# Kernel tuning notes

Measured on AMD Instinct MI355X. Metric: run time of the kernel, lower is better.

The kernel has to match this reference:

```python
import jax, jax.numpy as jnp
import numpy as np
import math

NH = 16
SIGMA = 1.5
KS = 7


def _gaussian_blur_16x16(x):
    # x: (N, 16, 16); torchvision GaussianBlur(7, 1.5) with reflect padding
    hx = jnp.arange(KS, dtype=x.dtype) - (KS - 1) / 2.0
    k1 = jnp.exp(-0.5 * (hx / SIGMA) ** 2)
    k1 = k1 / k1.sum()
    k2 = jnp.outer(k1, k1)[None, None]  # (1,1,7,7)
    pad = KS // 2
    xp = jnp.pad(x, ((0, 0), (pad, pad), (pad, pad)), mode='reflect')[:, None]
    y = jax.lax.conv_general_dilated(xp, k2, (1, 1), 'VALID')
    return y[:, 0]


def _normalize(w):
    mn, mx = w.min(), w.max()
    return (w - mn) / (mx - mn)


def _blurred_map(f, b_perm):
    # f, b_perm: (B, 256, 256)
    B = f.shape[0]
    bi = f * b_perm
    bi = bi.reshape(B * 256, 16, 16)
    bl = _gaussian_blur_16x16(bi)
    bl = jnp.clip(_normalize(bl), 0.0, 1.0)
    bl = bl.reshape(B, 256, 256)
    return bl * f * b_perm


def setup_inputs() -> dict:
    key = jax.random.key(0)
    ks = jax.random.split(key, 16)
    B, T, C = 4, 827, 1024
    inp = {
        'x': jax.random.normal(ks[0], (B, T, C), jnp.float32),
        'h': jax.random.normal(ks[1], (B, NH, 827, 827), jnp.float32) * 0.1,
        'f01': jax.random.uniform(ks[2], (B, 256, 256), jnp.float32),
        'f02': jax.random.uniform(ks[3], (B, 256, 256), jnp.float32),
        'f12': jax.random.uniform(ks[4], (B, 256, 256), jnp.float32),
        'b01': jax.random.uniform(ks[5], (B, 256, 256), jnp.float32),
        'b02': jax.random.uniform(ks[6], (B, 256, 256), jnp.float32),
        'b12': jax.random.uniform(ks[7], (B, 256, 256), jnp.float32),
        'Wq': jax.random.normal(ks[8], (C, C), jnp.float32) * 0.02,
        'bq': jnp.zeros((C,), jnp.float32),
        'Wk': jax.random.normal(ks[9], (C, C), jnp.float32) * 0.02,
        'bk': jnp.zeros((C,), jnp.float32),
        'Wv': jax.random.normal(ks[10], (C, C), jnp.float32) * 0.02,
        'bv': jnp.zeros((C,), jnp.float32),
        'Wp': jax.random.normal(ks[11], (C, C), jnp.float32) * 0.02,
        'bp': jnp.zeros((C,), jnp.float32),
    }
    return inp


def reference(x, h, f01, f02, f12, b01, b02, b12,
              Wq, bq, Wk, bk, Wv, bv, Wp, bp):
    B, T, C = x.shape
    hd = C // NH
    # QKV projections -> (B, NH, T, hd)
    def proj(W, b):
        return (x @ W + b).reshape(B, T, NH, hd).transpose(0, 2, 1, 3)
    q, k, v = proj(Wq, bq), proj(Wk, bk), proj(Wv, bv)

    att = jnp.einsum('bhtd,bhsd->bhts', q, k) * (1.0 / math.sqrt(hd))
    att = h[:, :, :T, :T] + att  # adaptive additive bias

    # bidirectional epipolar multiplicative masks with blur
    b01p = jnp.transpose(b01, (0, 2, 1))
    b02p = jnp.transpose(b02, (0, 2, 1))
    b12p = jnp.transpose(b12, (0, 2, 1))
    blur01 = _blurred_map(f01, b01p)[:, None]  # (B,1,256,256), broadcast over heads
    blur02 = _blurred_map(f02, b02p)[:, None]
    blur12 = _blurred_map(f12, b12p)[:, None]

    n1 = min(T - 285, 256)
    att = att.at[:, :, 285:285 + n1, 0:256].multiply(blur01[:, :, :n1])
    if T > 571:
        n2 = T - 571
        att = att.at[:, :, 571:T, 0:256].multiply(blur02[:, :, :n2])
        att = att.at[:, :, 571:T, 286:542].multiply(blur12[:, :, :n2])

    mask = jnp.tril(jnp.ones((T, T), dtype=bool))
    att = jnp.where(mask, att, -jnp.inf)
    att = jax.nn.softmax(att, axis=-1)

    y = jnp.einsum('bhts,bhsd->bhtd', att, v)
    y = y.transpose(0, 2, 1, 3).reshape(B, T, C)
    return y @ Wp + bp
```

## Files before the change

### kernel.cpp

```cpp
#include <hip/hip_runtime.h>
#include <math.h>

using bfrag8 = __attribute__((ext_vector_type(8))) short;
using facc4  = __attribute__((ext_vector_type(4))) float;

#define MFMA16(a,b,c) __builtin_amdgcn_mfma_f32_16x16x32_bf16((a),(b),(c),0,0,0)

#define T_SEQ 827
#define T_PAD 832
#define NHEAD 16
#define NEG_INF (-__builtin_inff())
#define CM_TOT 1179392

static __device__ __forceinline__ unsigned short f2bf(float f) {
    unsigned int x = __float_as_uint(f);
    unsigned int r = x + 0x7FFFu + ((x >> 16) & 1u);
    return (unsigned short)(r >> 16);
}

static __device__ __forceinline__ void gl16(const unsigned short* g, unsigned short* l) {
    __builtin_amdgcn_global_load_lds(
        (const __attribute__((address_space(1))) unsigned int*)g,
        (__attribute__((address_space(3))) unsigned int*)l,
        16, 0, 0);
}

__global__ __launch_bounds__(256) void k_front(const float* __restrict__ x,
                                               unsigned short* __restrict__ x_bf,
                                               float* __restrict__ cm,
                                               unsigned short* q, unsigned short* k,
                                               unsigned short* vT,
                                               const float* __restrict__ Wq,
                                               const float* __restrict__ Wk,
                                               const float* __restrict__ Wv,
                                               const float* __restrict__ Wp,
                                               unsigned short* __restrict__ Wt_out,
                                               const float* f01, const float* f02, const float* f12,
                                               const float* b01, const float* b02, const float* b12,
                                               float* __restrict__ bl,
                                               float* __restrict__ pmm) {
    __shared__ float tile[32][33];
    __shared__ float img[16][17], tmp[16][17];
    __shared__ float smn[4], smx[4];
    int bid = blockIdx.x, tid = threadIdx.x;

    if (bid < 3308) {
        int i = (bid * 256 + tid) * 4;
        float4 v = *reinterpret_cast<const float4*>(x + i);
        ushort4 o;
        o.x = f2bf(v.x); o.y = f2bf(v.y); o.z = f2bf(v.z); o.w = f2bf(v.w);
        *reinterpret_cast<ushort4*>(x_bf + i) = o;
    } else if (bid < 4460) {
        int base = (bid - 3308) * 1024 + tid * 4;
        if (base + 4 <= CM_TOT) {
            float4 one = {1.f, 1.f, 1.f, 1.f};
            *reinterpret_cast<float4*>(cm + base) = one;
        } else {
#pragma unroll
            for (int j = 0; j < 4; ++j)
                if (base + j < CM_TOT) cm[base + j] = 1.f;
        }
    } else if (bid < 4524) {
        int bh = bid - 4460;
        for (int i = tid; i < 320; i += 256) {
            int t = 827 + i / 64, d = i % 64;
            q[((size_t)bh * T_PAD + t) * 64 + d] = 0;
            k[((size_t)bh * T_PAD + t) * 64 + d] = 0;
        }
        for (int i = tid; i < 4096; i += 256) {
            int d = i >> 6, s = 768 + (i & 63);
            vT[((size_t)bh * 64 + d) * T_PAD + s] = 0;
        }
    } else if (bid < 8620) {
        int i = bid - 4524;
        int z = i >> 10, rem = i & 1023;
        int bx = rem & 31, by = rem >> 5;
        const float* W = (z == 0) ? Wq : (z == 1) ? Wk : (z == 2) ? Wv : Wp;
        unsigned short* Wt = Wt_out + (size_t)z * 1048576;
        int tx = tid & 31, ty0 = tid >> 5;
#pragma unroll
        for (int j = 0; j < 4; ++j) {
            int ty = ty0 + j * 8;
            tile[ty][tx] = W[(size_t)(by * 32 + ty) * 1024 + bx * 32 + tx];
        }
        __syncthreads();
#pragma unroll
        for (int j = 0; j < 4; ++j) {
            int ty = ty0 + j * 8;
            Wt[(size_t)(bx * 32 + ty) * 1024 + by * 32 + tx] = f2bf(tile[tx][ty]);
        }
    } else {
        int i = bid - 8620;
        int m = i >> 10, rem = i & 1023, b = rem >> 8, r = rem & 255;
        const float* f  = (m == 0) ? f01 : (m == 1) ? f02 : f12;
        const float* bm = (m == 0) ? b01 : (m == 1) ? b02 : b12;
        int ii = tid >> 4, j = tid & 15;

        float k1[7]; float ks = 0.f;
#pragma unroll
        for (int d = 0; d < 7; ++d) { float hx = (float)d - 3.f; k1[d] = expf(-0.5f * hx * hx / 2.25f); ks += k1[d]; }
#pragma unroll
        for (int d = 0; d < 7; ++d) k1[d] /= ks;

        size_t idx = (size_t)b * 65536 + (size_t)r * 256 + tid;
        float bi = f[idx] * bm[(size_t)b * 65536 + (size_t)tid * 256 + r];
        img[ii][j] = bi;
        __syncthreads();
        float ha = 0.f;
#pragma unroll
        for (int d = 0; d < 7; ++d) { int p = j - 3 + d; p = p < 0 ? -p : (p > 15 ? 30 - p : p); ha += k1[d] * img[ii][p]; }
        tmp[ii][j] = ha;
        __syncthreads();
        float v = 0.f;
#pragma unroll
        for (int d = 0; d < 7; ++d) { int p = ii - 3 + d; p = p < 0 ? -p : (p > 15 ? 30 - p : p); v += k1[d] * tmp[p][j]; }
        bl[(size_t)m * 262144 + idx] = v;

        float mn = v, mx = v;
#pragma unroll
        for (int off = 32; off; off >>= 1) { mn = fminf(mn, __shfl_xor(mn, off)); mx = fmaxf(mx, __shfl_xor(mx, off)); }
        int wid = tid >> 6, lane = tid & 63;
        if (lane == 0) { smn[wid] = mn; smx[wid] = mx; }
        __syncthreads();
        if (tid == 0) {
            mn = fminf(fminf(smn[0], smn[1]), fminf(smn[2], smn[3]));
            mx = fmaxf(fmaxf(smx[0], smx[1]), fmaxf(smx[2], smx[3]));
            pmm[2 * i]     = mn;
            pmm[2 * i + 1] = mx;
        }
    }
}

__global__ __launch_bounds__(256) void k_gemm_qkv(const unsigned short* __restrict__ A,
                                              const unsigned short* __restrict__ Bt,
                                              const float* __restrict__ b0, const float* __restrict__ b1,
                                              const float* __restrict__ b2,
                                              unsigned short* __restrict__ qo, unsigned short* __restrict__ ko,
                                              unsigned short* __restrict__ vo, int M,
                                              const float* f01, const float* f02, const float* f12,
                                              const float* b01, const float* b02, const float* b12,
                                              const float* __restrict__ bl,
                                              const float* __restrict__ pmm,
                                              float* __restrict__ cm) {
    __shared__ unsigned short As[2][4096];
    __shared__ unsigned short Bs[2][4096];
    int bid = blockIdx.x, tid = threadIdx.x;

    if (bid >= 624) {
        int i = bid - 624;
        int m = i >> 10, rem = i & 1023, b = rem >> 8, r = rem & 255;
        float mn = __builtin_inff(), mx = 0.f;
        for (int kk = tid; kk < 1024; kk += 256) {
            int e = m * 1024 + kk;
            mn = fminf(mn, pmm[2 * e]);
            mx = fmaxf(mx, pmm[2 * e + 1]);
        }
#pragma unroll
        for (int off = 32; off; off >>= 1) { mn = fminf(mn, __shfl_xor(mn, off)); mx = fmaxf(mx, __shfl_xor(mx, off)); }
        float* fs = reinterpret_cast<float*>(&As[0][0]);
        int wid = tid >> 6, lane = tid & 63;
        if (lane == 0) { fs[wid] = mn; fs[4 + wid] = mx; }
        __syncthreads();
        mn = fminf(fminf(fs[0], fs[1]), fminf(fs[2], fs[3]));
        mx = fmaxf(fmaxf(fs[4], fs[5]), fmaxf(fs[6], fs[7]));

        const float* f  = (m == 0) ? f01 : (m == 1) ? f02 : f12;
        const float* bm = (m == 0) ? b01 : (m == 1) ? b02 : b12;
        size_t idx = (size_t)b * 65536 + (size_t)r * 256 + tid;
        float w = (bl[(size_t)m * 262144 + idx] - mn) / (mx - mn);
        w = fminf(fmaxf(w, 0.f), 1.f);
        float val = w * f[idx] * bm[(size_t)b * 65536 + (size_t)tid * 256 + r];
        int row = (m == 0) ? r : r + 286;
        int col = (m == 2) ? tid + 286 : tid;
        cm[((size_t)b * 542 + row) * 544 + col] = val;
        return;
    }

    int swz = (bid & 7) * 78 + (bid >> 3);
    int m0 = (swz % 26) * 128, n0 = (swz / 26) * 128;
    int wid = tid >> 6, lane = tid & 63;
    int g = lane >> 4, l15 = lane & 15;
    int wm = wid >> 1, wn = wid & 1;
    facc4 acc[4][4] = {};

    int ar0 = m0 + (tid >> 2); if (ar0 > M - 1) ar0 = M - 1;
    int ar1 = m0 + 64 + (tid >> 2); if (ar1 > M - 1) ar1 = M - 1;
    const unsigned short* Ap0 = A + (size_t)ar0 * 1024 + (tid & 3) * 8;
    const unsigned short* Ap1 = A + (size_t)ar1 * 1024 + (tid & 3) * 8;
    const unsigned short* Bp0 = Bt + (size_t)(n0 + (tid >> 2)) * 1024 + (tid & 3) * 8;
    const unsigned short* Bp1 = Bp0 + (size_t)64 * 1024;

    auto stage = [&](int koff, int buf) {
        gl16(Ap0 + koff, &As[buf][0] + (wid << 9));
        gl16(Ap1 + koff, &As[buf][0] + (wid << 9) + 2048);
        gl16(Bp0 + koff, &Bs[buf][0] + (wid << 9));
        gl16(Bp1 + koff, &Bs[buf][0] + (wid << 9) + 2048);
    };

    stage(0, 0);
    for (int k0 = 0; k0 < 32; ++k0) {
        int cur = k0 & 1;
        bool morek = (k0 + 1 < 32);
        if (morek) {
            stage((k0 + 1) * 32, cur ^ 1);
            asm volatile("s_waitcnt vmcnt(4)" ::: "memory");
        } else {
            asm volatile("s_waitcnt vmcnt(0)" ::: "memory");
        }
        __builtin_amdgcn_s_barrier();
        __builtin_amdgcn_sched_barrier(0);

        bfrag8 af[4], bf[4];
#pragma unroll
        for (int mi = 0; mi < 4; ++mi)
            af[mi] = *reinterpret_cast<const bfrag8*>(&As[cur][(wm * 64 + mi * 16 + l15) * 32 + g * 8]);
#pragma unroll
        for (int ni = 0; ni < 4; ++ni)
            bf[ni] = *reinterpret_cast<const bfrag8*>(&Bs[cur][(wn * 64 + ni * 16 + l15) * 32 + g * 8]);
        __builtin_amdgcn_s_setprio(1);
#pragma unroll
        for (int mi = 0; mi < 4; ++mi)
#pragma unroll
            for (int ni = 0; ni < 4; ++ni)
                acc[mi][ni] = MFMA16(af[mi], bf[ni], acc[mi][ni]);
        __builtin_amdgcn_s_setprio(0);

        __builtin_amdgcn_sched_barrier(0);
        if (morek) __builtin_amdgcn_s_barrier();
    }

    int which = n0 >> 10;
    const float* bb = (which == 0 ? b0 : (which == 1 ? b1 : b2));
#pragma unroll
    for (int mi = 0; mi < 4; ++mi)
#pragma unroll
        for (int ni = 0; ni < 4; ++ni)
#pragma unroll
            for (int r = 0; r < 4; ++r) {
                int row = m0 + wm * 64 + mi * 16 + g * 4 + r;
                if (row >= M) continue;
                int col = n0 + wn * 64 + ni * 16 + l15;
                float v = acc[mi][ni][r] + bb[col & 1023];
                int b = row / T_SEQ, t = row - b * T_SEQ;
                int cc = col & 1023;
                int hh = cc >> 6, d = cc & 63;
                size_t bh = (size_t)(b * NHEAD + hh);
                if (which == 0) {
                    qo[(bh * T_PAD + t) * 64 + d] = f2bf(v);
                } else if (which == 1) {
                    int du = (((d >> 3) ^ (t & 7)) << 3) | (d & 7);
                    ko[(bh * T_PAD + t) * 64 + du] = f2bf(v);
                } else {
                    int sl = t & 63;
                    int su = (((sl >> 3) ^ (d & 7)) << 3) | (t & 7);
                    vo[(bh * 64 + d) * T_PAD + (t - sl) + su] = f2bf(v);
                }
            }
}

__global__ __launch_bounds__(256) void k_proj64(const unsigned short* __restrict__ A,
                                                const unsigned short* __restrict__ Bt,
                                                const float* __restrict__ bias,
                                                float* __restrict__ out, int M) {
    __shared__ unsigned short As[2048];
    __shared__ unsigned short Bs[2048];
    int bid = blockIdx.x, tid = threadIdx.x;
    int swz = (bid & 7) * 104 + (bid >> 3);
    int m0 = (swz % 52) * 64, n0 = (swz / 52) * 64;
    int wid = tid >> 6, lane = tid & 63;
    int g = lane >> 4, l15 = lane & 15;
    int wm = wid >> 1, wn = wid & 1;
    facc4 acc[2][2] = {};

    int ar = m0 + (tid >> 2); if (ar > M - 1) ar = M - 1;
    const unsigned short* Ap = A + (size_t)ar * 1024 + (tid & 3) * 8;
    const unsigned short* Bp = Bt + (size_t)(n0 + (tid >> 2)) * 1024 + (tid & 3) * 8;
    unsigned short* asw = As + (wid << 9);
    unsigned short* bsw = Bs + (wid << 9);

    for (int k0 = 0; k0 < 1024; k0 += 32) {
        if (k0) __syncthreads();
        gl16(Ap + k0, asw);
        gl16(Bp + k0, bsw);
        __syncthreads();
        bfrag8 af[2], bf[2];
#pragma unroll
        for (int mi = 0; mi < 2; ++mi)
            af[mi] = *reinterpret_cast<const bfrag8*>(&As[(wm * 32 + mi * 16 + l15) * 32 + g * 8]);
#pragma unroll
        for (int ni = 0; ni < 2; ++ni)
            bf[ni] = *reinterpret_cast<const bfrag8*>(&Bs[(wn * 32 + ni * 16 + l15) * 32 + g * 8]);
#pragma unroll
        for (int mi = 0; mi < 2; ++mi)
#pragma unroll
            for (int ni = 0; ni < 2; ++ni)
                acc[mi][ni] = MFMA16(af[mi], bf[ni], acc[mi][ni]);
    }

#pragma unroll
    for (int mi = 0; mi < 2; ++mi)
#pragma unroll
        for (int ni = 0; ni < 2; ++ni)
#pragma unroll
            for (int r = 0; r < 4; ++r) {
                int row = m0 + wm * 32 + mi * 16 + g * 4 + r;
                if (row >= M) continue;
                int col = n0 + wn * 32 + ni * 16 + l15;
                out[(size_t)row * 1024 + col] = acc[mi][ni][r] + bias[col];
            }
}

__global__ __launch_bounds__(256, 3) void k_attn(const unsigned short* __restrict__ qb,
                                              const unsigned short* __restrict__ kb,
                                              const unsigned short* __restrict__ vT,
                                              const float* __restrict__ h,
                                              const float* __restrict__ cm,
                                              unsigned short* __restrict__ y) {
    int blk0 = blockIdx.x;
    int blk = (blk0 & 7) * 104 + (blk0 >> 3);
    int bh = blk / 13;
    int qt = 12 - (blk % 13);
    int b = bh >> 4, hh = bh & 15;
    int tid = threadIdx.x, wid = tid >> 6, lane = tid & 63;
    int g = lane >> 4, l15 = lane & 15;
    int t0 = qt * 64 + wid * 16;
    int t = t0 + l15;
    int tcl = t > 826 ? 826 : t;
    int ntiles = qt + 1;

    __shared__ unsigned short Ks[2][4096];
    __shared__ unsigned short Vs[2][4096];
    __shared__ unsigned short Ps[4][1024];
    unsigned short* pw = &Ps[wid][0];

    const unsigned short* Kbase = kb + (size_t)bh * T_PAD * 64;
    const unsigned short* Vbase = vT + (size_t)bh * 64 * T_PAD;
    const float* hrow = h + (size_t)bh * T_SEQ * T_SEQ + (size_t)tcl * T_SEQ;
    int rt = t - 285; rt = rt < 0 ? 0 : (rt > 541 ? 541 : rt);
    const float* cmrow = cm + ((size_t)b * 542 + rt) * 544;
    bool tm = (t >= 285);

    size_t qrow = ((size_t)bh * T_PAD + t) * 64 + g * 8;
    bfrag8 aq0 = *reinterpret_cast<const bfrag8*>(qb + qrow);
    bfrag8 aq1 = *reinterpret_cast<const bfrag8*>(qb + qrow + 32);

    auto stage = [&](int s0, int buf) {
        const unsigned short* kt = Kbase + (size_t)s0 * 64;
        unsigned short* kd = &Ks[buf][0] + (wid << 9);
        gl16(kt + tid * 8, kd);
        gl16(kt + 2048 + tid * 8, kd + 2048);
        const unsigned short* vt = Vbase + s0;
        unsigned short* vd = &Vs[buf][0] + (wid << 9);
        gl16(vt + (size_t)(tid >> 3) * T_PAD + (tid & 7) * 8, vd);
        gl16(vt + (size_t)((tid >> 3) + 32) * T_PAD + (tid & 7) * 8, vd + 2048);
    };

    auto loadh_h = [&](int s0t, float* hd) {
#pragma unroll
        for (int nt = 0; nt < 4; ++nt) {
            int sb = s0t + nt * 16 + 4 * g;
#pragma unroll
            for (int j = 0; j < 4; ++j) {
                int a = sb + j;
                int ac = a > 826 ? 826 : a;
                float hx = hrow[ac];
                hd[nt * 4 + j] = (a <= tcl) ? hx : 0.f;
            }
        }
    };

    auto loadm = [&](int s0t, float* mvd) {
#pragma unroll
        for (int nt = 0; nt < 4; ++nt) {
            int sb = s0t + nt * 16 + 4 * g;
            float m4[4];
            if (tm && sb <= 540) {
                __builtin_memcpy(m4, cmrow + sb, 16);
            } else {
#pragma unroll
                for (int j = 0; j < 4; ++j) m4[j] = 1.f;
            }
#pragma unroll
            for (int j = 0; j < 4; ++j) mvd[nt * 4 + j] = m4[j];
        }
    };

    float m_r = NEG_INF, l_r = 0.f;
    facc4 acc[4] = {};
    float hv[16], mv[16], hn[16];
    stage(0, 0);
    loadh_h(0, hv);
    loadm(0, mv);

    for (int it = 0; it < ntiles; ++it) {
        int cur = it & 1, s0 = it * 64;
        bool more = (it + 1 < ntiles);
        bool diag = !more;

        if (more) {
            stage(s0 + 64, cur ^ 1);
            loadh_h(s0 + 64, hn);
            __builtin_amdgcn_sched_barrier(0);
            asm volatile("s_waitcnt vmcnt(20)" ::: "memory");
        } else {
            asm volatile("s_waitcnt vmcnt(0)" ::: "memory");
        }
        __builtin_amdgcn_s_barrier();
        __builtin_amdgcn_sched_barrier(0);

        facc4 sf[4] = {};
        __builtin_amdgcn_s_setprio(1);
#pragma unroll
        for (int nt = 0; nt < 4; ++nt) {
            int row = nt * 16 + l15;
            const unsigned short* kp = &Ks[cur][row * 64];
            bfrag8 k0 = *reinterpret_cast<const bfrag8*>(kp + ((g ^ (row & 7)) << 3));
            bfrag8 k1 = *reinterpret_cast<const bfrag8*>(kp + (((4 + g) ^ (row & 7)) << 3));
            sf[nt] = MFMA16(k0, aq0, sf[nt]);
            sf[nt] = MFMA16(k1, aq1, sf[nt]);
        }
        __builtin_amdgcn_s_setprio(0);

        float vmax = NEG_INF;
#pragma unroll
        for (int nt = 0; nt < 4; ++nt)
#pragma unroll
            for (int r = 0; r < 4; ++r) {
                float val = fmaf(sf[nt][r], 0.125f, hv[nt * 4 + r]) * mv[nt * 4 + r];
                if (diag) {
                    int s = s0 + nt * 16 + 4 * g + r;
                    val = (s <= tcl) ? val : NEG_INF;
                }
                sf[nt][r] = val;
                vmax = fmaxf(vmax, val);
            }

        if (more) loadm(s0 + 64, mv);

        vmax = fmaxf(vmax, __shfl_xor(vmax, 16));
        vmax = fmaxf(vmax, __shfl_xor(vmax, 32));

        bool noresc = __all(vmax <= m_r + 6.0f);
        float mnew = fmaxf(m_r, vmax);
        float mexp = noresc ? m_r : mnew;

        float ps = 0.f;
#pragma unroll
        for (int nt = 0; nt < 4; ++nt)
#pragma unroll
            for (int r = 0; r < 4; ++r) {
                float p = __expf(sf[nt][r] - mexp);
                sf[nt][r] = p;
                ps += p;
            }
        ps += __shfl_xor(ps, 16);
        ps += __shfl_xor(ps, 32);

#pragma unroll
        for (int nt = 0; nt < 4; ++nt) {
            unsigned u0, u1;
            asm("v_cvt_pk_bf16_f32 %0, %1, %2" : "=v"(u0) : "v"(sf[nt][0]), "v"(sf[nt][1]));
            asm("v_cvt_pk_bf16_f32 %0, %1, %2" : "=v"(u1) : "v"(sf[nt][2]), "v"(sf[nt][3]));
            int el = (l15 * 64 + nt * 16 + 4 * g) ^ ((l15 & 7) << 3);
            uint2 uu; uu.x = u0; uu.y = u1;
            *reinterpret_cast<uint2*>(&pw[el]) = uu;
        }

        if (!noresc) {
            float scale = __expf(m_r - mnew);
            l_r = l_r * scale + ps;
#pragma unroll
            for (int r = 0; r < 4; ++r) {
                float sc = __int_as_float(__builtin_amdgcn_ds_bpermute((4 * g + r) * 4, __float_as_int(scale)));
#pragma unroll
                for (int dt = 0; dt < 4; ++dt) acc[dt][r] *= sc;
            }
            m_r = mnew;
        } else {
            l_r += ps;
        }

        __builtin_amdgcn_s_setprio(1);
#pragma unroll
        for (int c2 = 0; c2 < 2; ++c2) {
            int ela = (l15 * 64 + c2 * 32 + 8 * g) ^ ((l15 & 7) << 3);
            bfrag8 ap = *reinterpret_cast<const bfrag8*>(&pw[ela]);
#pragma unroll
            for (int dt = 0; dt < 4; ++dt) {
                int row = dt * 16 + l15;
                bfrag8 vf = *reinterpret_cast<const bfrag8*>(&Vs[cur][row * 64 + (((c2 * 4 + g) ^ (row & 7)) << 3)]);
                acc[dt] = MFMA16(ap, vf, acc[dt]);
            }
        }
        __builtin_amdgcn_s_setprio(0);

        __builtin_amdgcn_sched_barrier(0);
        __builtin_amdgcn_s_barrier();
        if (more) {
#pragma unroll
            for (int i2 = 0; i2 < 16; ++i2) hv[i2] = hn[i2];
        }
    }

    float linv = 1.0f / l_r;
#pragma unroll
    for (int r = 0; r < 4; ++r) {
        float li = __int_as_float(__builtin_amdgcn_ds_bpermute((4 * g + r) * 4, __float_as_int(linv)));
        int tt = t0 + 4 * g + r;
        if (tt < T_SEQ) {
#pragma unroll
            for (int dt = 0; dt < 4; ++dt)
                y[((size_t)(b * T_SEQ) + tt) * 1024 + hh * 64 + dt * 16 + l15] = f2bf(acc[dt][r] * li);
        }
    }
}

extern "C" void kernel_launch(void* const* d_in, const int* in_sizes, int n_in,
                              void* d_out, int out_size, void* d_ws, size_t ws_size,
                              hipStream_t stream) {
    const float* x   = (const float*)d_in[0];
    const float* h   = (const float*)d_in[1];
    const float* f01 = (const float*)d_in[2];
    const float* f02 = (const float*)d_in[3];
    const float* f12 = (const float*)d_in[4];
    const float* b01 = (const float*)d_in[5];
    const float* b02 = (const float*)d_in[6];
    const float* b12 = (const float*)d_in[7];
    const float* Wq  = (const float*)d_in[8];
    const float* bq  = (const float*)d_in[9];
    const float* Wk  = (const float*)d_in[10];
    const float* bk  = (const float*)d_in[11];
    const float* Wv  = (const float*)d_in[12];
    const float* bv  = (const float*)d_in[13];
    const float* Wp  = (const float*)d_in[14];
    const float* bp  = (const float*)d_in[15];

    char* ws = (char*)d_ws;
    float* pmm    = (float*)(ws + 256);
    float* bl     = (float*)(ws + 256 + 24576);
    float* cmb    = (float*)(ws + 256 + 24576 + 3145728);
    unsigned short* x_bf  = (unsigned short*)(ws + 256 + 24576 + 3145728 + 4717568);
    unsigned short* WtQKV = x_bf + (size_t)3308 * 1024;
    unsigned short* WtP   = WtQKV + (size_t)3072 * 1024;
    unsigned short* q_bf  = WtP + (size_t)1024 * 1024;
    unsigned short* k_bf  = q_bf + (size_t)64 * T_PAD * 64;
    unsigned short* vTb   = k_bf + (size_t)64 * T_PAD * 64;
    unsigned short* y_bf  = vTb  + (size_t)64 * T_PAD * 64;

    k_front<<<11692, 256, 0, stream>>>(x, x_bf, cmb, q_bf, k_bf, vTb,
                                       Wq, Wk, Wv, Wp, WtQKV,
                                       f01, f02, f12, b01, b02, b12, bl, pmm);
    k_gemm_qkv<<<3696, 256, 0, stream>>>(x_bf, WtQKV, bq, bk, bv, q_bf, k_bf, vTb, 3308,
                                         f01, f02, f12, b01, b02, b12, bl, pmm, cmb);
    k_attn<<<832, 256, 0, stream>>>(q_bf, k_bf, vTb, h, cmb, y_bf);
    k_proj64<<<832, 256, 0, stream>>>(y_bf, WtP, bp, (float*)d_out, 3308);
}
```

Before: 163.4 us.

## Stage attention bias tiles into LDS via async global-to-LDS loads

The additive bias h is now copied into a double-buffered, XOR-swizzled shared-memory tile with global_load_lds instead of per-lane scalar register loads. The diagonal tile still loads h directly into registers. The pipeline is reordered so the next K/V/h stage is issued after the barrier and the second barrier is dropped, and mask loads move to the end of the iteration. The extra 32KB of LDS forces the occupancy hint down from 3 to 2 blocks per CU. This trades occupancy and synchronisation safety for coalesced bias loads and fewer vector registers.

```diff
diff --git a/kernel.cpp b/kernel.cpp
--- a/kernel.cpp
+++ b/kernel.cpp
@@ -18,7 +18,7 @@
     return (unsigned short)(r >> 16);
 }
 
-static __device__ __forceinline__ void gl16(const unsigned short* g, unsigned short* l) {
+static __device__ __forceinline__ void gl16(const void* g, void* l) {
     __builtin_amdgcn_global_load_lds(
         (const __attribute__((address_space(1))) unsigned int*)g,
         (__attribute__((address_space(3))) unsigned int*)l,
@@ -310,7 +310,7 @@
             }
 }
 
-__global__ __launch_bounds__(256, 3) void k_attn(const unsigned short* __restrict__ qb,
+__global__ __launch_bounds__(256, 2) void k_attn(const unsigned short* __restrict__ qb,
                                               const unsigned short* __restrict__ kb,
                                               const unsigned short* __restrict__ vT,
                                               const float* __restrict__ h,
@@ -326,16 +326,18 @@
     int t0 = qt * 64 + wid * 16;
     int t = t0 + l15;
     int tcl = t > 826 ? 826 : t;
-    int ntiles = qt + 1;
+    int nt_ = qt + 1;
 
     __shared__ unsigned short Ks[2][4096];
     __shared__ unsigned short Vs[2][4096];
     __shared__ unsigned short Ps[4][1024];
+    __shared__ float Hs[2][64][64];
     unsigned short* pw = &Ps[wid][0];
 
     const unsigned short* Kbase = kb + (size_t)bh * T_PAD * 64;
     const unsigned short* Vbase = vT + (size_t)bh * 64 * T_PAD;
-    const float* hrow = h + (size_t)bh * T_SEQ * T_SEQ + (size_t)tcl * T_SEQ;
+    const float* hbase = h + (size_t)bh * (size_t)(T_SEQ * T_SEQ);
+    const float* hrow  = hbase + (size_t)tcl * T_SEQ;
     int rt = t - 285; rt = rt < 0 ? 0 : (rt > 541 ? 541 : rt);
     const float* cmrow = cm + ((size_t)b * 542 + rt) * 544;
     bool tm = (t >= 285);
@@ -344,7 +346,7 @@
     bfrag8 aq0 = *reinterpret_cast<const bfrag8*>(qb + qrow);
     bfrag8 aq1 = *reinterpret_cast<const bfrag8*>(qb + qrow + 32);
 
-    auto stage = [&](int s0, int buf) {
+    auto stage_kv = [&](int s0, int buf) {
         const unsigned short* kt = Kbase + (size_t)s0 * 64;
         unsigned short* kd = &Ks[buf][0] + (wid << 9);
         gl16(kt + tid * 8, kd);
@@ -355,58 +357,66 @@
         gl16(vt + (size_t)((tid >> 3) + 32) * T_PAD + (tid & 7) * 8, vd + 2048);
     };
 
-    auto loadh_h = [&](int s0t, float* hd) {
+    auto stage_h = [&](int s0, int buf) {
+        int pc = lane & 15;
+#pragma unroll
+        for (int c = 0; c < 4; ++c) {
+            int rl = c * 4 + (lane >> 4);
+            int trow = qt * 64 + wid * 16 + rl;
+            if (trow > 826) trow = 826;
+            int gc = pc ^ (rl & 7);
+            const float* src = hbase + (size_t)trow * T_SEQ + (s0 + gc * 4);
+            gl16(src, &Hs[buf][wid * 16 + c * 4][0]);
+        }
+    };
+
+    auto loadm = [&](int s0t, float* mvd) {
 #pragma unroll
         for (int nt = 0; nt < 4; ++nt) {
             int sb = s0t + nt * 16 + 4 * g;
-#pragma unroll
-            for (int j = 0; j < 4; ++j) {
-                int a = sb + j;
-                int ac = a > 826 ? 826 : a;
-                float hx = hrow[ac];
-                hd[nt * 4 + j] = (a <= tcl) ? hx : 0.f;
-            }
+            int scl = sb > 540 ? 540 : sb;
+            float m4[4];
+            __builtin_memcpy(m4, cmrow + scl, 16);
+#pragma unroll
+            for (int j = 0; j < 4; ++j) mvd[nt * 4 + j] = m4[j];
         }
     };
 
-    auto loadm = [&](int s0t, float* mvd) {
+    auto loadh_diag = [&](int s0t, float* hd) {
 #pragma unroll
         for (int nt = 0; nt < 4; ++nt) {
             int sb = s0t + nt * 16 + 4 * g;
-            float m4[4];
-            if (tm && sb <= 540) {
-                __builtin_memcpy(m4, cmrow + sb, 16);
-            } else {
-#pragma unroll
-                for (int j = 0; j < 4; ++j) m4[j] = 1.f;
-            }
-#pragma unroll
-            for (int j = 0; j < 4; ++j) mvd[nt * 4 + j] = m4[j];
+#pragma unroll
+            for (int j = 0; j < 4; ++j) {
+                int a = sb + j; if (a > 826) a = 826;
+                hd[nt * 4 + j] = hrow[a];
+            }
         }
     };
 
     float m_r = NEG_INF, l_r = 0.f;
     facc4 acc[4] = {};
-    float hv[16], mv[16], hn[16];
-    stage(0, 0);
-    loadh_h(0, hv);
+    float mv[16], hd[16];
+
+    stage_kv(0, 0);
+    if (nt_ > 1) stage_h(0, 0);
     loadm(0, mv);
-
-    for (int it = 0; it < ntiles; ++it) {
+    if (nt_ == 1) loadh_diag(0, hd);
+
+    for (int it = 0; it < nt_; ++it) {
         int cur = it & 1, s0 = it * 64;
-        bool more = (it + 1 < ntiles);
-        bool diag = !more;
-
-        if (more) {
-            stage(s0 + 64, cur ^ 1);
-            loadh_h(s0 + 64, hn);
-            __builtin_amdgcn_sched_barrier(0);
-            asm volatile("s_waitcnt vmcnt(20)" ::: "memory");
-        } else {
-            asm volatile("s_waitcnt vmcnt(0)" ::: "memory");
-        }
+        bool last = (it == nt_ - 1);
+        bool diag = last;
+
+        if (!last) { asm volatile("s_waitcnt vmcnt(4)" ::: "memory"); }
+        else       { asm volatile("s_waitcnt vmcnt(0)" ::: "memory"); }
         __builtin_amdgcn_s_barrier();
         __builtin_amdgcn_sched_barrier(0);
+
+        if (!last) {
+            stage_kv(s0 + 64, cur ^ 1);
+            if (it + 1 < nt_ - 1) stage_h(s0 + 64, cur ^ 1);
+        }
 
         facc4 sf[4] = {};
         __builtin_amdgcn_s_setprio(1);
@@ -423,19 +433,30 @@
 
         float vmax = NEG_INF;
 #pragma unroll
-        for (int nt = 0; nt < 4; ++nt)
-#pragma unroll
-            for (int r = 0; r < 4; ++r) {
-                float val = fmaf(sf[nt][r], 0.125f, hv[nt * 4 + r]) * mv[nt * 4 + r];
+        for (int nt = 0; nt < 4; ++nt) {
+            float h4[4];
+            if (diag) {
+#pragma unroll
+                for (int j = 0; j < 4; ++j) h4[j] = hd[nt * 4 + j];
+            } else {
+                float4 hq = *reinterpret_cast<const float4*>(
+                    &Hs[cur][wid * 16 + l15][(((nt * 4 + g) ^ (l15 & 7)) << 2)]);
+                h4[0] = hq.x; h4[1] = hq.y; h4[2] = hq.z; h4[3] = hq.w;
+            }
+            int sbc = s0 + nt * 16 + 4 * g;
+            bool useM = tm && (sbc <= 540);
+#pragma unroll
+            for (int j = 0; j < 4; ++j) {
+                float mveff = useM ? mv[nt * 4 + j] : 1.0f;
+                float val = fmaf(sf[nt][j], 0.125f, h4[j]) * mveff;
                 if (diag) {
-                    int s = s0 + nt * 16 + 4 * g + r;
+                    int s = sbc + j;
                     val = (s <= tcl) ? val : NEG_INF;
                 }
-                sf[nt][r] = val;
+                sf[nt][j] = val;
                 vmax = fmaxf(vmax, val);
             }
-
-        if (more) loadm(s0 + 64, mv);
+        }
 
         vmax = fmaxf(vmax, __shfl_xor(vmax, 16));
         vmax = fmaxf(vmax, __shfl_xor(vmax, 32));
@@ -494,11 +515,9 @@
         }
         __builtin_amdgcn_s_setprio(0);
 
-        __builtin_amdgcn_sched_barrier(0);
-        __builtin_amdgcn_s_barrier();
-        if (more) {
-#pragma unroll
-            for (int i2 = 0; i2 < 16; ++i2) hv[i2] = hn[i2];
+        if (!last) {
+            loadm(s0 + 64, mv);
+            if (it == nt_ - 2) loadh_diag(s0 + 64, hd);
         }
     }
 
```

Result: faster. 141.0 us (-13.7%).
